# Kernel optimization log

Hardware: AMD Instinct MI355X
Metric: run time of the kernel (lower is better)

Reference implementation:

```python
import jax, jax.numpy as jnp
import numpy as np


def setup_inputs() -> dict:
    key = jax.random.key(0)
    k0, k1, k2, k3, k4 = jax.random.split(key, 5)
    T, B, I, H = 1024, 128, 256, 256
    x = jax.random.normal(k0, (T, B, I), dtype=jnp.float32)
    h0 = jax.random.normal(k1, (1, B, H), dtype=jnp.float32)
    # prepacked transposed weights, gate order [r|z|n] along the 3H axis
    wihT = jax.random.normal(k2, (I, 3 * H), dtype=jnp.float32) * 0.05
    whhT = jax.random.normal(k3, (H, 3 * H), dtype=jnp.float32) * 0.05
    b = jax.random.normal(k4, (3 * H,), dtype=jnp.float32) * 0.05  # fused b_ih + b_hh
    return {"x": x, "h0": h0, "wihT": wihT, "whhT": whhT, "b": b}


def reference(x, h0, wihT, whhT, b):
    # Single-layer GRU recurrence, matching the fused CUDA kernel math:
    #   r = sigmoid(x Wir + h Whr + b_r)
    #   z = sigmoid(x Wiz + h Whz + b_z)
    #   h' = (1 - z) * n + z * h
    H = h0.shape[-1]
    br, bz, bn = b[:H], b[H:2 * H], b[2 * H:]

    def step(h, xt):
        gi = xt @ wihT   # (B, 3H)
        gh = h @ whhT    # (B, 3H)
        r = jax.nn.sigmoid(gi[:, :H] + gh[:, :H] + br)
        z = jax.nn.sigmoid(gi[:, H:2 * H] + gh[:, H:2 * H] + bz)
        n = jnp.tanh(gi[:, 2 * H:] + bn + r * gh[:, 2 * H:])
        h_new = (1.0 - z) * n + z * h
        return h_new, None

    h_final, _ = jax.lax.scan(step, h0[0], x)  # scan over T
    return h_final[None]  # (1, B, H)
```

## Files before the change

### kernel.cpp

```cpp
#include <hip/hip_runtime.h>
#include <hip/hip_fp16.h>

#define TT 1024
#define BB 128
#define II 256
#define HH 256
#define NG 768

__device__ __align__(16) unsigned short g_xbf[(size_t)TT * BB * II];
__device__ __align__(16) unsigned short g_wihB[NG * II];
__device__ __align__(16) _Float16       g_gi[(size_t)TT * BB * NG];

typedef __attribute__((ext_vector_type(8))) short    bfrag;
typedef __attribute__((ext_vector_type(8))) _Float16 hfrag;
typedef __attribute__((ext_vector_type(4))) float    f32x4;

__device__ __forceinline__ unsigned short f2bf(float f) {
    unsigned u = __float_as_uint(f);
    return (unsigned short)((u + 0x7fffu + ((u >> 16) & 1u)) >> 16);
}

__global__ void cvt_x_kernel(const float* __restrict__ x) {
    const int n4 = TT * BB * II / 4;
    for (int i = blockIdx.x * blockDim.x + threadIdx.x; i < n4;
         i += gridDim.x * blockDim.x) {
        float4 v = reinterpret_cast<const float4*>(x)[i];
        ushort4 o;
        o.x = f2bf(v.x); o.y = f2bf(v.y); o.z = f2bf(v.z); o.w = f2bf(v.w);
        reinterpret_cast<ushort4*>(g_xbf)[i] = o;
    }
}

__global__ void cvt_wih_kernel(const float* __restrict__ wihT) {
    const int n = blockIdx.x;
    const int k = threadIdx.x;
    g_wihB[n * II + k] = f2bf(wihT[k * NG + n]);
}

__global__ void __launch_bounds__(256) gi_gemm_kernel(const float* __restrict__ bias) {
    __shared__ unsigned short Ab[128 * 32];
    __shared__ unsigned short Bb[128 * 32];
    const int tid = threadIdx.x;
    const int mt = blockIdx.x / 6, nt = blockIdx.x % 6;
    const int m0 = mt * 128, n0 = nt * 128;
    const int l = tid & 63, w = tid >> 6;
    const int wr = w >> 1, wc = w & 1;
    const int srow = tid >> 2, scol = (tid & 3) * 8;

    f32x4 acc[4][4] = {};

    for (int ks = 0; ks < 8; ++ks) {
        const int k0 = ks * 32;
        __syncthreads();
        #pragma unroll
        for (int c = 0; c < 2; ++c) {
            const int row = c * 64 + srow;
            *reinterpret_cast<uint4*>(&Ab[row * 32 + scol]) =
                *reinterpret_cast<const uint4*>(&g_xbf[(size_t)(m0 + row) * II + k0 + scol]);
            *reinterpret_cast<uint4*>(&Bb[row * 32 + scol]) =
                *reinterpret_cast<const uint4*>(&g_wihB[(n0 + row) * II + k0 + scol]);
        }
        __syncthreads();
        bfrag af[4], bf[4];
        #pragma unroll
        for (int i = 0; i < 4; ++i) {
            af[i] = *reinterpret_cast<const bfrag*>(
                        &Ab[(wr * 64 + i * 16 + (l & 15)) * 32 + (l >> 4) * 8]);
            bf[i] = *reinterpret_cast<const bfrag*>(
                        &Bb[(wc * 64 + i * 16 + (l & 15)) * 32 + (l >> 4) * 8]);
        }
        #pragma unroll
        for (int mi = 0; mi < 4; ++mi)
            #pragma unroll
            for (int ni = 0; ni < 4; ++ni)
                acc[mi][ni] = __builtin_amdgcn_mfma_f32_16x16x32_bf16(
                                  af[mi], bf[ni], acc[mi][ni], 0, 0, 0);
    }
    #pragma unroll
    for (int mi = 0; mi < 4; ++mi) {
        const int grow = m0 + wr * 64 + mi * 16 + (l >> 4) * 4;
        #pragma unroll
        for (int ni = 0; ni < 4; ++ni) {
            const int gcol = n0 + wc * 64 + ni * 16 + (l & 15);
            const float bv = bias[gcol];
            #pragma unroll
            for (int q = 0; q < 4; ++q)
                g_gi[(size_t)(grow + q) * NG + gcol] = (_Float16)(acc[mi][ni][q] + bv);
        }
    }
}

#define MF(A, B, C) __builtin_amdgcn_mfma_f32_16x16x32_f16((A), (B), (C), 0, 0, 0)

#define LDB1(NAME, GATE, TB, KT)                                            \
    hfrag NAME;                                                             \
    _Pragma("unroll")                                                       \
    for (int e = 0; e < 8; ++e)                                             \
        NAME[e] = (_Float16)whhT[(size_t)((KT) * 32 + g8 + e) * NG          \
                                 + (GATE) * HH + (TB) + ln15];              \
    asm("" : "+a"(NAME));

#define DECL8(P, GATE, I, TB)                                               \
    LDB1(P##I##_0, GATE, TB, 0) LDB1(P##I##_1, GATE, TB, 1)                 \
    LDB1(P##I##_2, GATE, TB, 2) LDB1(P##I##_3, GATE, TB, 3)                 \
    LDB1(P##I##_4, GATE, TB, 4) LDB1(P##I##_5, GATE, TB, 5)                 \
    LDB1(P##I##_6, GATE, TB, 6) LDB1(P##I##_7, GATE, TB, 7)

#define KST(KT)                                                             \
    {                                                                       \
        const hfrag A = *reinterpret_cast<const hfrag*>(hl + (KT) * 32 + g8); \
        aR0 = MF(A, BR0_##KT, aR0); aR1 = MF(A, BR1_##KT, aR1);             \
        aR2 = MF(A, BR2_##KT, aR2); aR3 = MF(A, BR3_##KT, aR3);             \
        aZ0 = MF(A, BZ0_##KT, aZ0); aZ1 = MF(A, BZ1_##KT, aZ1);             \
        aZ2 = MF(A, BZ2_##KT, aZ2); aZ3 = MF(A, BZ3_##KT, aZ3);             \
        aN0 = MF(A, BN0_##KT, aN0); aN1 = MF(A, BN1_##KT, aN1);             \
        aN2 = MF(A, BN2_##KT, aN2); aN3 = MF(A, BN3_##KT, aN3);             \
    }

__global__ void __launch_bounds__(256, 1)
__attribute__((amdgpu_waves_per_eu(1, 1)))
gru_rec_kernel(
    const float* __restrict__ h0, const float* __restrict__ whhT,
    float* __restrict__ out)
{
    __shared__ __align__(16) _Float16 hbuf[2][HH];

    const int t    = threadIdx.x;
    const int b    = blockIdx.x;
    const int w    = t >> 6;
    const int l    = t & 63;
    const int ln15 = l & 15;
    const int gq   = l >> 4;
    const int g8   = gq * 8;
    const int tb0  = (4 * w + 0) * 16, tb1 = (4 * w + 1) * 16;
    const int tb2  = (4 * w + 2) * 16, tb3 = (4 * w + 3) * 16;

    DECL8(BR, 0, 0, tb0) DECL8(BR, 0, 1, tb1)
    DECL8(BR, 0, 2, tb2) DECL8(BR, 0, 3, tb3)
    DECL8(BZ, 1, 0, tb0) DECL8(BZ, 1, 1, tb1)
    DECL8(BZ, 1, 2, tb2) DECL8(BZ, 1, 3, tb3)
    DECL8(BN, 2, 0, tb0) DECL8(BN, 2, 1, tb1)
    DECL8(BN, 2, 2, tb2) DECL8(BN, 2, 3, tb3)

    float hp = h0[b * HH + t];
    hbuf[0][t] = (_Float16)hp;
    __syncthreads();

    for (int ts = 0; ts < TT; ++ts) {
        const _Float16* hl  = hbuf[ts & 1];
        _Float16*       hn_ = hbuf[(ts & 1) ^ 1];

        const _Float16* gb = g_gi + ((size_t)ts * BB + b) * NG + t;
        const float gR = (float)gb[0];
        const float gZ = (float)gb[256];
        const float gN = (float)gb[512];

        f32x4 aR0 = {0.f,0.f,0.f,0.f}, aR1 = {0.f,0.f,0.f,0.f};
        f32x4 aR2 = {0.f,0.f,0.f,0.f}, aR3 = {0.f,0.f,0.f,0.f};
        f32x4 aZ0 = {0.f,0.f,0.f,0.f}, aZ1 = {0.f,0.f,0.f,0.f};
        f32x4 aZ2 = {0.f,0.f,0.f,0.f}, aZ3 = {0.f,0.f,0.f,0.f};
        f32x4 aN0 = {0.f,0.f,0.f,0.f}, aN1 = {0.f,0.f,0.f,0.f};
        f32x4 aN2 = {0.f,0.f,0.f,0.f}, aN3 = {0.f,0.f,0.f,0.f};
        KST(0) KST(1) KST(2) KST(3) KST(4) KST(5) KST(6) KST(7)

        const float sR = gq == 0 ? aR0[0] : gq == 1 ? aR1[0] : gq == 2 ? aR2[0] : aR3[0];
        const float sZ = gq == 0 ? aZ0[0] : gq == 1 ? aZ1[0] : gq == 2 ? aZ2[0] : aZ3[0];
        const float sN = gq == 0 ? aN0[0] : gq == 1 ? aN1[0] : gq == 2 ? aN2[0] : aN3[0];

        const float r  = 1.f / (1.f + __expf(-(sR + gR)));
        const float z  = 1.f / (1.f + __expf(-(sZ + gZ)));
        const float e  = __expf(2.f * (gN + r * sN));
        const float n  = 1.f - 2.f / (e + 1.f);
        const float hv = (1.f - z) * n + z * hp;

        hp = hv;
        hn_[t] = (_Float16)hv;
        if (ts == TT - 1) out[b * HH + t] = hv;
        __syncthreads();
    }
}

extern "C" void kernel_launch(void* const* d_in, const int* in_sizes, int n_in,
                              void* d_out, int out_size, void* d_ws, size_t ws_size,
                              hipStream_t stream) {
    const float* x    = (const float*)d_in[0];
    const float* h0   = (const float*)d_in[1];
    const float* wihT = (const float*)d_in[2];
    const float* whhT = (const float*)d_in[3];
    const float* bias = (const float*)d_in[4];
    float*       out  = (float*)d_out;

    cvt_x_kernel<<<2048, 256, 0, stream>>>(x);
    cvt_wih_kernel<<<NG, 256, 0, stream>>>(wihT);
    gi_gemm_kernel<<<1024 * 6, 256, 0, stream>>>(bias);
    gru_rec_kernel<<<BB, 256, 0, stream>>>(h0, whhT, out);
}
```

Baseline: 1.478 ms.

## Split GRU recurrence across eight waves with two column tiles each

The recurrent kernel now launches 512 threads per batch row instead of 256. Each wave holds register-resident Whh fragments for 2 column tiles per gate instead of 4. This halves the serial MFMA chain each wave runs per timestep and reduces per-wave register pressure, aiming to shorten the latency-bound recurrence step. In exchange, every step's barrier now has to synchronise more waves, and half the lanes redundantly compute and write the same hidden element.

```diff
diff --git a/kernel.cpp b/kernel.cpp
--- a/kernel.cpp
+++ b/kernel.cpp
@@ -92,80 +92,67 @@
 
 #define MF(A, B, C) __builtin_amdgcn_mfma_f32_16x16x32_f16((A), (B), (C), 0, 0, 0)
 
-#define LDB1(NAME, GATE, TB, KT)                                            \
+#define LDB1(NAME, CB, KT)                                                  \
     hfrag NAME;                                                             \
     _Pragma("unroll")                                                       \
     for (int e = 0; e < 8; ++e)                                             \
-        NAME[e] = (_Float16)whhT[(size_t)((KT) * 32 + g8 + e) * NG          \
-                                 + (GATE) * HH + (TB) + ln15];              \
+        NAME[e] = (_Float16)whhT[(size_t)((KT) * 32 + g8 + e) * NG + (CB) + c]; \
     asm("" : "+a"(NAME));
 
-#define DECL8(P, GATE, I, TB)                                               \
-    LDB1(P##I##_0, GATE, TB, 0) LDB1(P##I##_1, GATE, TB, 1)                 \
-    LDB1(P##I##_2, GATE, TB, 2) LDB1(P##I##_3, GATE, TB, 3)                 \
-    LDB1(P##I##_4, GATE, TB, 4) LDB1(P##I##_5, GATE, TB, 5)                 \
-    LDB1(P##I##_6, GATE, TB, 6) LDB1(P##I##_7, GATE, TB, 7)
+#define DECL8(P, CB)                                                        \
+    LDB1(P##_0, CB, 0) LDB1(P##_1, CB, 1) LDB1(P##_2, CB, 2)                \
+    LDB1(P##_3, CB, 3) LDB1(P##_4, CB, 4) LDB1(P##_5, CB, 5)                \
+    LDB1(P##_6, CB, 6) LDB1(P##_7, CB, 7)
 
 #define KST(KT)                                                             \
     {                                                                       \
         const hfrag A = *reinterpret_cast<const hfrag*>(hl + (KT) * 32 + g8); \
         aR0 = MF(A, BR0_##KT, aR0); aR1 = MF(A, BR1_##KT, aR1);             \
-        aR2 = MF(A, BR2_##KT, aR2); aR3 = MF(A, BR3_##KT, aR3);             \
         aZ0 = MF(A, BZ0_##KT, aZ0); aZ1 = MF(A, BZ1_##KT, aZ1);             \
-        aZ2 = MF(A, BZ2_##KT, aZ2); aZ3 = MF(A, BZ3_##KT, aZ3);             \
         aN0 = MF(A, BN0_##KT, aN0); aN1 = MF(A, BN1_##KT, aN1);             \
-        aN2 = MF(A, BN2_##KT, aN2); aN3 = MF(A, BN3_##KT, aN3);             \
     }
 
-__global__ void __launch_bounds__(256, 1)
-__attribute__((amdgpu_waves_per_eu(1, 1)))
-gru_rec_kernel(
+__global__ void __launch_bounds__(512, 1) gru_rec_kernel(
     const float* __restrict__ h0, const float* __restrict__ whhT,
     float* __restrict__ out)
 {
     __shared__ __align__(16) _Float16 hbuf[2][HH];
 
-    const int t    = threadIdx.x;
-    const int b    = blockIdx.x;
-    const int w    = t >> 6;
-    const int l    = t & 63;
-    const int ln15 = l & 15;
-    const int gq   = l >> 4;
-    const int g8   = gq * 8;
-    const int tb0  = (4 * w + 0) * 16, tb1 = (4 * w + 1) * 16;
-    const int tb2  = (4 * w + 2) * 16, tb3 = (4 * w + 3) * 16;
+    const int t   = threadIdx.x;
+    const int b   = blockIdx.x;
+    const int w   = t >> 6;
+    const int l   = t & 63;
+    const int c   = l & 15;
+    const int sel = l >> 4;
+    const int g8  = sel * 8;
+    const int cw  = w * 16;
+    const int j   = (sel & 1) * 128 + cw + c;
 
-    DECL8(BR, 0, 0, tb0) DECL8(BR, 0, 1, tb1)
-    DECL8(BR, 0, 2, tb2) DECL8(BR, 0, 3, tb3)
-    DECL8(BZ, 1, 0, tb0) DECL8(BZ, 1, 1, tb1)
-    DECL8(BZ, 1, 2, tb2) DECL8(BZ, 1, 3, tb3)
-    DECL8(BN, 2, 0, tb0) DECL8(BN, 2, 1, tb1)
-    DECL8(BN, 2, 2, tb2) DECL8(BN, 2, 3, tb3)
+    DECL8(BR0, cw)        DECL8(BR1, 128 + cw)
+    DECL8(BZ0, 256 + cw)  DECL8(BZ1, 384 + cw)
+    DECL8(BN0, 512 + cw)  DECL8(BN1, 640 + cw)
 
-    float hp = h0[b * HH + t];
-    hbuf[0][t] = (_Float16)hp;
+    float hp = h0[b * HH + j];
+    hbuf[0][j] = (_Float16)hp;
     __syncthreads();
 
     for (int ts = 0; ts < TT; ++ts) {
         const _Float16* hl  = hbuf[ts & 1];
         _Float16*       hn_ = hbuf[(ts & 1) ^ 1];
 
-        const _Float16* gb = g_gi + ((size_t)ts * BB + b) * NG + t;
+        const _Float16* gb = g_gi + ((size_t)ts * BB + b) * NG + j;
         const float gR = (float)gb[0];
         const float gZ = (float)gb[256];
         const float gN = (float)gb[512];
 
         f32x4 aR0 = {0.f,0.f,0.f,0.f}, aR1 = {0.f,0.f,0.f,0.f};
-        f32x4 aR2 = {0.f,0.f,0.f,0.f}, aR3 = {0.f,0.f,0.f,0.f};
         f32x4 aZ0 = {0.f,0.f,0.f,0.f}, aZ1 = {0.f,0.f,0.f,0.f};
-        f32x4 aZ2 = {0.f,0.f,0.f,0.f}, aZ3 = {0.f,0.f,0.f,0.f};
         f32x4 aN0 = {0.f,0.f,0.f,0.f}, aN1 = {0.f,0.f,0.f,0.f};
-        f32x4 aN2 = {0.f,0.f,0.f,0.f}, aN3 = {0.f,0.f,0.f,0.f};
         KST(0) KST(1) KST(2) KST(3) KST(4) KST(5) KST(6) KST(7)
 
-        const float sR = gq == 0 ? aR0[0] : gq == 1 ? aR1[0] : gq == 2 ? aR2[0] : aR3[0];
-        const float sZ = gq == 0 ? aZ0[0] : gq == 1 ? aZ1[0] : gq == 2 ? aZ2[0] : aZ3[0];
-        const float sN = gq == 0 ? aN0[0] : gq == 1 ? aN1[0] : gq == 2 ? aN2[0] : aN3[0];
+        const float sR = (sel & 1) ? aR1[0] : aR0[0];
+        const float sZ = (sel & 1) ? aZ1[0] : aZ0[0];
+        const float sN = (sel & 1) ? aN1[0] : aN0[0];
 
         const float r  = 1.f / (1.f + __expf(-(sR + gR)));
         const float z  = 1.f / (1.f + __expf(-(sZ + gZ)));
@@ -174,8 +161,8 @@
         const float hv = (1.f - z) * n + z * hp;
 
         hp = hv;
-        hn_[t] = (_Float16)hv;
-        if (ts == TT - 1) out[b * HH + t] = hv;
+        hn_[j] = (_Float16)hv;
+        if (ts == TT - 1) out[b * HH + j] = hv;
         __syncthreads();
     }
 }
@@ -193,5 +180,5 @@
     cvt_x_kernel<<<2048, 256, 0, stream>>>(x);
     cvt_wih_kernel<<<NG, 256, 0, stream>>>(wihT);
     gi_gemm_kernel<<<1024 * 6, 256, 0, stream>>>(bias);
-    gru_rec_kernel<<<BB, 256, 0, stream>>>(h0, whhT, out);
+    gru_rec_kernel<<<BB, 512, 0, stream>>>(h0, whhT, out);
 }
```

Result: faster. 1.345 ms (-9.0%).
